# Performance work log

Hardware: AMD Instinct MI355X
Metric: run time of the kernel (lower is better)

## Reference

```python
import jax, jax.numpy as jnp
import numpy as np

EPS_CB = 1e-6   # ConvBlock BN eps (partial(nn.BatchNorm2d, eps=1e-6))
EPS_BN = 1e-5   # default nn.BatchNorm2d / BatchNorm1d eps


def conv2d(x, w, stride=1, pad=0):
    return jax.lax.conv_general_dilated(
        x, w, (stride, stride), [(pad, pad), (pad, pad)],
        dimension_numbers=('NCHW', 'OIHW', 'NCHW'))


def bn2d(x, g, b, m, v, eps):
    inv = (g / jnp.sqrt(v + eps)).reshape(1, -1, 1, 1)
    return (x - m.reshape(1, -1, 1, 1)) * inv + b.reshape(1, -1, 1, 1)


def setup_inputs() -> dict:
    key = jax.random.key(0)
    ks = iter(jax.random.split(key, 40))
    B, C, H, W = 16, 512, 64, 64
    K = 64                 # num_codes (hard-coded to 64 in __init__)
    c4 = C // 4            # bottleneck width in ConvBlock (expansion=4)

    def w_(shape, scale=0.05):
        return jax.random.normal(next(ks), shape, jnp.float32) * scale

    def bnp(n):
        return (jax.random.uniform(next(ks), (n,), jnp.float32, 0.5, 1.5),  # gamma
                w_((n,), 0.05),                                            # beta
                w_((n,), 0.05),                                            # running mean
                jax.random.uniform(next(ks), (n,), jnp.float32, 0.5, 1.5)) # running var

    g1, b1, m1, v1 = bnp(c4)
    g2, b2, m2, v2 = bnp(c4)
    g3, b3, m3, v3 = bnp(C)
    gr, br, mr, vr = bnp(C)
    gl, bl, ml, vl = bnp(C)
    ge, be, me, ve = bnp(K)

    std = 1.0 / np.sqrt(K * C)
    inp = {
        'x': jax.random.normal(next(ks), (B, C, H, W), jnp.float32),
        # ConvBlock
        'w1': w_((c4, C, 1, 1)), 'g1': g1, 'b1': b1, 'm1': m1, 'v1': v1,
        'w2': w_((c4, c4, 3, 3)), 'g2': g2, 'b2': b2, 'm2': m2, 'v2': v2,
        'w3': w_((C, c4, 1, 1)), 'g3': g3, 'b3': b3, 'm3': m3, 'v3': v3,
        'wr': w_((C, C, 1, 1)), 'gr': gr, 'br': br, 'mr': mr, 'vr': vr,
        # LVC 1x1 conv + BN2d
        'wl': w_((C, C, 1, 1)), 'gl': gl, 'bl': bl, 'ml': ml, 'vl': vl,
        # Encoding
        'codewords': jax.random.uniform(next(ks), (K, C), jnp.float32, -std, std),
        'scale': jax.random.uniform(next(ks), (K,), jnp.float32, -1.0, 0.0),
        # BN1d over codes
        'ge': ge, 'be': be, 'me': me, 've': ve,
        # fc gate
        'wfc': w_((C, C)), 'bfc': w_((C,), 0.05),
    }
    return inp


def lvc_forward(x, w1, g1, b1, m1, v1, w2, g2, b2, m2, v2, w3, g3, b3, m3, v3,
                wr, gr, br, mr, vr, wl, gl, bl, ml, vl, codewords, scale,
                ge, be, me, ve, wfc, bfc):
    # ---- ConvBlock (bottleneck with 1x1 residual), eval-mode BN ----
    h = jax.nn.relu(bn2d(conv2d(x, w1), g1, b1, m1, v1, EPS_CB))
    h = jax.nn.relu(bn2d(conv2d(h, w2, pad=1), g2, b2, m2, v2, EPS_CB))
    h = jax.nn.relu(bn2d(conv2d(h, w3), g3, b3, m3, v3, EPS_CB))
    res = bn2d(conv2d(x, wr), gr, br, mr, vr, EPS_CB)
    x1 = h + res                                   # (B, C, H, W)

    # ---- LVC: 1x1 conv + BN + ReLU ----
    y = jax.nn.relu(bn2d(conv2d(x1, wl), gl, bl, ml, vl, EPS_BN))

    # ---- Encoding: scaled L2 -> softmax over codes -> aggregate ----
    B, C, H, W = y.shape
    xf = y.reshape(B, C, H * W).transpose(0, 2, 1)     # (B, N, C)
    x_sq = jnp.sum(xf * xf, axis=-1, keepdims=True)    # (B, N, 1)
    c_sq = jnp.sum(codewords * codewords, axis=-1)     # (K,)
    xc = jnp.einsum('bnc,kc->bnk', xf, codewords)      # (B, N, K)
    dist = scale * (x_sq - 2.0 * xc + c_sq)            # (B, N, K)
    A = jax.nn.softmax(dist, axis=2)                   # assignment weights
    # sum_n A[b,n,k] * (x[b,n,:] - codewords[k,:])  -> (B, K, C)
    enc = jnp.einsum('bnk,bnc->bkc', A, xf) - A.sum(axis=1)[..., None] * codewords

    # ---- BN1d over num_codes dim + ReLU + mean over codes ----
    inv = (ge / jnp.sqrt(ve + EPS_BN)).reshape(1, -1, 1)
    enc = (enc - me.reshape(1, -1, 1)) * inv + be.reshape(1, -1, 1)
    en = jax.nn.relu(enc).mean(axis=1)                 # (B, C)

    # ---- SE-style gate ----
    gam = jax.nn.sigmoid(en @ wfc.T + bfc)             # (B, C)
    gate = gam.reshape(B, C, 1, 1)
    return jax.nn.relu(x1 + x1 * gate)


def reference(x, w1, g1, b1, m1, v1, w2, g2, b2, m2, v2, w3, g3, b3, m3, v3,
              wr, gr, br, mr, vr, wl, gl, bl, ml, vl, codewords, scale,
              ge, be, me, ve, wfc, bfc):
    return lvc_forward(x, w1, g1, b1, m1, v1, w2, g2, b2, m2, v2,
                       w3, g3, b3, m3, v3, wr, gr, br, mr, vr,
                       wl, gl, bl, ml, vl, codewords, scale,
                       ge, be, me, ve, wfc, bfc)
```

## Files before the change

### kernel.cpp

```cpp
#include <hip/hip_runtime.h>
#include <math.h>

typedef float f32x4 __attribute__((ext_vector_type(4)));
typedef short s16x8 __attribute__((ext_vector_type(8)));
typedef unsigned short u16x4 __attribute__((ext_vector_type(4)));

#define HW 4096
#define CCH 512
#define NK 64
#define EPAD 136

#define C_XB   0ULL
#define C_H2   67108864ULL
#define C_H1P  83886080ULL
#define C_X1B  83886080ULL
#define C_YB   0ULL
#define C_AHI  67108864ULL
#define C_ALO  75497472ULL
#define C_ASUM 150994944ULL
#define C_GAM  150999040ULL
#define C_MISC 151031808ULL
#define C_W1F  151048192ULL
#define C_W2F  151179264ULL
#define C_W3B  151474176ULL
#define C_WRB  151605248ULL
#define C_WLB  152129536ULL
#define C_PE   152653824ULL
#define C_CWH  161042432ULL
#define C_CWL  161107968ULL

#define MS_S1 0
#define MS_T1 128
#define MS_S2 256
#define MS_T2 384
#define MS_S3 512
#define MS_T3 1024
#define MS_SR 1536
#define MS_TR 2048
#define MS_SL 2560
#define MS_TL 3072
#define MS_SE 3584
#define MS_TE 3648
#define MS_CSQ 3712

__device__ __forceinline__ float b2f(unsigned short u) {
  unsigned int x = ((unsigned int)u) << 16;
  return __builtin_bit_cast(float, x);
}
__device__ __forceinline__ unsigned short f2b(float f) {
  unsigned int i = __builtin_bit_cast(unsigned int, f);
  i += 0x7fffu + ((i >> 16) & 1u);
  return (unsigned short)(i >> 16);
}

__global__ void prep_kernel(
    const float* __restrict__ g1, const float* __restrict__ b1, const float* __restrict__ m1, const float* __restrict__ v1,
    const float* __restrict__ g2, const float* __restrict__ b2, const float* __restrict__ m2, const float* __restrict__ v2,
    const float* __restrict__ g3, const float* __restrict__ b3, const float* __restrict__ m3, const float* __restrict__ v3,
    const float* __restrict__ gr, const float* __restrict__ br, const float* __restrict__ mr, const float* __restrict__ vr,
    const float* __restrict__ gl, const float* __restrict__ bl, const float* __restrict__ ml, const float* __restrict__ vl,
    const float* __restrict__ ge, const float* __restrict__ be, const float* __restrict__ me, const float* __restrict__ ve,
    const float* __restrict__ cw, float* __restrict__ misc)
{
  const int t = threadIdx.x;
  if (t < 128) {
    float s = g1[t] * rsqrtf(v1[t] + 1e-6f);
    misc[MS_S1 + t] = s; misc[MS_T1 + t] = b1[t] - m1[t] * s;
    s = g2[t] * rsqrtf(v2[t] + 1e-6f);
    misc[MS_S2 + t] = s; misc[MS_T2 + t] = b2[t] - m2[t] * s;
  }
  for (int c = t; c < 512; c += 256) {
    float s = g3[c] * rsqrtf(v3[c] + 1e-6f);
    misc[MS_S3 + c] = s; misc[MS_T3 + c] = b3[c] - m3[c] * s;
    s = gr[c] * rsqrtf(vr[c] + 1e-6f);
    misc[MS_SR + c] = s; misc[MS_TR + c] = br[c] - mr[c] * s;
    s = gl[c] * rsqrtf(vl[c] + 1e-5f);
    misc[MS_SL + c] = s; misc[MS_TL + c] = bl[c] - ml[c] * s;
  }
  if (t < 64) {
    float s = ge[t] * rsqrtf(ve[t] + 1e-5f);
    misc[MS_SE + t] = s; misc[MS_TE + t] = be[t] - me[t] * s;
    float acc = 0.f;
    for (int c = 0; c < 512; ++c) { float v = cw[t * 512 + c]; acc += v * v; }
    misc[MS_CSQ + t] = acc;
  }
}

__global__ void fold_bf16_kernel(const float* __restrict__ w, const float* __restrict__ s,
                                 unsigned short* __restrict__ out, int total, int kper)
{
  int i = blockIdx.x * 256 + threadIdx.x;
  if (i < total) out[i] = f2b(w[i] * s[i / kper]);
}

__global__ void fold_w2_kernel(const float* __restrict__ w2, const float* __restrict__ s,
                               unsigned short* __restrict__ out)
{
  int j = blockIdx.x * 256 + threadIdx.x;
  if (j < 147456) {
    int m = j / 1152, r = j - m * 1152;
    int tp = r >> 7, ci = r & 127;
    out[j] = f2b(w2[m * 1152 + ci * 9 + tp] * s[m]);
  }
}

__global__ void fold_cw_kernel(const float* __restrict__ cw,
                               unsigned short* __restrict__ ch, unsigned short* __restrict__ cl)
{
  int i = blockIdx.x * 256 + threadIdx.x;
  if (i < 32768) {
    const float v = cw[i];
    const unsigned short hi = f2b(v);
    ch[i] = hi;
    cl[i] = f2b(v - b2f(hi));
  }
}

__global__ __launch_bounds__(256) void tr_kernel(const float* __restrict__ x,
                                                 unsigned short* __restrict__ xb)
{
  __shared__ float T[64][65];
  const int b = blockIdx.z, c0 = blockIdx.y * 64, n0 = blockIdx.x * 64;
  const int t = threadIdx.x;
  const int rr = t >> 4, cc = (t & 15) * 4;
#pragma unroll
  for (int rep = 0; rep < 4; ++rep) {
    const int cr = rep * 16 + rr;
    const float4 v = *(const float4*)(x + ((size_t)(b * 512 + c0 + cr)) * 4096 + n0 + cc);
    T[cr][cc + 0] = v.x; T[cr][cc + 1] = v.y; T[cr][cc + 2] = v.z; T[cr][cc + 3] = v.w;
  }
  __syncthreads();
#pragma unroll
  for (int rep = 0; rep < 4; ++rep) {
    const int nr = rep * 16 + rr;
    u16x4 o;
    o[0] = f2b(T[cc + 0][nr]); o[1] = f2b(T[cc + 1][nr]);
    o[2] = f2b(T[cc + 2][nr]); o[3] = f2b(T[cc + 3][nr]);
    *(u16x4*)(xb + ((size_t)(b * 4096 + n0 + nr)) * 512 + c0 + cc) = o;
  }
}

template<int BMODE>
__device__ __forceinline__ void run_phase(
    const unsigned short* __restrict__ Wp,
    const unsigned short* __restrict__ Xb,
    const int K, const int tid, const int n0,
    unsigned short* __restrict__ As, unsigned short* __restrict__ Bs,
    f32x4 acc[4][4])
{
  const int lane = tid & 63;
  const int wv = tid >> 6, wm = wv >> 1, wn = wv & 1;

  const int ko = tid & 3;
  const int r0 = tid >> 2;
  const int r1 = 64 + r0;

  const unsigned short* aS0 = Wp + (size_t)r0 * K + ko * 8;
  const unsigned short* aS1 = Wp + (size_t)r1 * K + ko * 8;
  const int slot0 = (((r0 >> 4) * 64) + ko * 16 + (r0 & 15)) * 8;
  const int slot1 = (((r1 >> 4) * 64) + ko * 16 + (r1 & 15)) * 8;

  const unsigned short* bS0 = nullptr;
  const unsigned short* bS1 = nullptr;
  size_t bBase0 = 0, bBase1 = 0;
  if constexpr (BMODE == 0) {
    bS0 = Xb + (size_t)(n0 + r0) * K + ko * 8;
    bS1 = Xb + (size_t)(n0 + r1) * K + ko * 8;
  } else {
    const int pg0 = n0 + r0, pg1 = n0 + r1;
    bBase0 = (size_t)((pg0 >> 6) * 66 + (pg0 & 63)) * 128 + ko * 8;
    bBase1 = (size_t)((pg1 >> 6) * 66 + (pg1 & 63)) * 128 + ko * 8;
  }

  s16x8 a0, a1, b0, b1;
  auto LOADC = [&](int kt) {
    __builtin_memcpy(&a0, aS0 + kt, 16);
    __builtin_memcpy(&a1, aS1 + kt, 16);
    if constexpr (BMODE == 0) {
      __builtin_memcpy(&b0, bS0 + kt, 16);
      __builtin_memcpy(&b1, bS1 + kt, 16);
    } else {
      const int tap = kt >> 7;
      const int ky = tap / 3, kx = tap - ky * 3;
      const int off = (ky * 66 + kx) * 128 + (kt & 127);
      __builtin_memcpy(&b0, Xb + bBase0 + off, 16);
      __builtin_memcpy(&b1, Xb + bBase1 + off, 16);
    }
  };

  LOADC(0);
  *(s16x8*)(As + slot0) = a0; *(s16x8*)(As + slot1) = a1;
  *(s16x8*)(Bs + slot0) = b0; *(s16x8*)(Bs + slot1) = b1;
  __syncthreads();

  int cur = 0;
  for (int kt = 0; kt < K; kt += 32) {
    const bool more = (kt + 32) < K;
    if (more) LOADC(kt + 32);

    const unsigned short* Ac = As + cur * 4096;
    const unsigned short* Bc = Bs + cur * 4096;
    s16x8 afr[4], bfr[4];
#pragma unroll
    for (int i = 0; i < 4; ++i)
      afr[i] = *(const s16x8*)(Ac + (size_t)((wm * 4 + i) * 64 + lane) * 8);
#pragma unroll
    for (int j = 0; j < 4; ++j)
      bfr[j] = *(const s16x8*)(Bc + (size_t)((wn * 4 + j) * 64 + lane) * 8);
#pragma unroll
    for (int i = 0; i < 4; ++i)
#pragma unroll
      for (int j = 0; j < 4; ++j)
        acc[i][j] = __builtin_amdgcn_mfma_f32_16x16x32_bf16(afr[i], bfr[j], acc[i][j], 0, 0, 0);

    if (more) {
      const int nx = (cur ^ 1) * 4096;
      *(s16x8*)(As + nx + slot0) = a0; *(s16x8*)(As + nx + slot1) = a1;
      *(s16x8*)(Bs + nx + slot0) = b0; *(s16x8*)(Bs + nx + slot1) = b1;
    }
    __syncthreads();
    cur ^= 1;
  }
}

template<int BMODE, bool DUAL>
__global__ __launch_bounds__(256) void mgemm_kernel(
    const unsigned short* __restrict__ W0, const unsigned short* __restrict__ X0,
    const int K0, const long long xbs0,
    const unsigned short* __restrict__ W1, const unsigned short* __restrict__ X1,
    const int Kp1, const long long xbs1,
    const float* __restrict__ biasMid, const float* __restrict__ biasOut,
    const int omode, const int reluF, const int ldm,
    unsigned short* __restrict__ outB, const long long obsB)
{
  __shared__ __align__(16) unsigned short smem[128 * EPAD];
  unsigned short* As = smem;
  unsigned short* Bs = smem + 8192;

  const int tid = threadIdx.x;
  const int b = blockIdx.z;
  const int n0 = blockIdx.x * 128;
  const int m0 = blockIdx.y * 128;
  const int lane = tid & 63, wv = tid >> 6, wm = wv >> 1, wn = wv & 1;
  const int q = lane >> 4, mm = lane & 15;

  f32x4 acc[4][4];
#pragma unroll
  for (int i = 0; i < 4; ++i)
#pragma unroll
    for (int j = 0; j < 4; ++j) acc[i][j] = (f32x4){0.f, 0.f, 0.f, 0.f};

  run_phase<BMODE>(W0 + (size_t)m0 * K0, X0 + (size_t)b * xbs0, K0, tid, n0, As, Bs, acc);

  if constexpr (DUAL) {
#pragma unroll
    for (int i = 0; i < 4; ++i) {
      const int mb = m0 + wm * 64 + i * 16 + q * 4;
#pragma unroll
      for (int r = 0; r < 4; ++r) {
        const float bm = biasMid[mb + r];
#pragma unroll
        for (int j = 0; j < 4; ++j) acc[i][j][r] = fmaxf(acc[i][j][r] + bm, 0.f);
      }
    }
    run_phase<0>(W1 + (size_t)m0 * Kp1, X1 + (size_t)b * xbs1, Kp1, tid, n0, As, Bs, acc);
  }

  __syncthreads();
  if (omode == 3) {
#pragma unroll
    for (int i = 0; i < 4; ++i) {
      const int chb = wm * 64 + i * 16 + q * 4;
#pragma unroll
      for (int r = 0; r < 4; ++r) {
        const float bo = biasOut[m0 + chb + r];
#pragma unroll
        for (int j = 0; j < 4; ++j) {
          const int px = wn * 64 + j * 16 + mm;
          float v = acc[i][j][r] + bo;
          if (reluF) v = fmaxf(v, 0.f);
          smem[(size_t)(chb + r) * EPAD + px] = f2b(v);
        }
      }
    }
    __syncthreads();
    const int ch = tid >> 1, half = tid & 1;
    const unsigned short* src = smem + (size_t)ch * EPAD + half * 64;
    unsigned short* dst = outB + (size_t)b * obsB + (size_t)(m0 + ch) * HW + n0 + half * 64;
#pragma unroll
    for (int r = 0; r < 8; ++r) {
      s16x8 v;
      __builtin_memcpy(&v, src + r * 8, 16);
      *(s16x8*)(dst + r * 8) = v;
    }
  } else {
#pragma unroll
    for (int i = 0; i < 4; ++i) {
      const int chb = wm * 64 + i * 16 + q * 4;
      float bo[4];
#pragma unroll
      for (int r = 0; r < 4; ++r) bo[r] = biasOut[m0 + chb + r];
#pragma unroll
      for (int j = 0; j < 4; ++j) {
        const int px = wn * 64 + j * 16 + mm;
        u16x4 o;
#pragma unroll
        for (int r = 0; r < 4; ++r) {
          float v = acc[i][j][r] + bo[r];
          if (reluF) v = fmaxf(v, 0.f);
          o[r] = f2b(v);
        }
        *(u16x4*)(smem + (size_t)px * EPAD + chb) = o;
      }
    }
    __syncthreads();
    const int px = tid >> 1, half = tid & 1;
    const unsigned short* src = smem + (size_t)px * EPAD + half * 64;
    size_t dstoff;
    if (omode == 1) {
      dstoff = (size_t)b * obsB + (size_t)(n0 + px) * ldm + m0 + half * 64;
    } else {
      const int hp = ((n0 + px) >> 6) + 1, wp = ((n0 + px) & 63) + 1;
      dstoff = (size_t)b * obsB + ((size_t)hp * 66 + wp) * 128 + m0 + half * 64;
    }
    unsigned short* dst = outB + dstoff;
#pragma unroll
    for (int r = 0; r < 8; ++r) {
      s16x8 v;
      __builtin_memcpy(&v, src + r * 8, 16);
      *(s16x8*)(dst + r * 8) = v;
    }
  }
}

__global__ __launch_bounds__(256) void assign_mfma_kernel(
    const unsigned short* __restrict__ Yv,
    const unsigned short* __restrict__ cwh, const unsigned short* __restrict__ cwl,
    const float* __restrict__ scale, const float* __restrict__ misc,
    unsigned short* __restrict__ Ahi, unsigned short* __restrict__ Alo)
{
  __shared__ __align__(16) unsigned short Bt[64][36];
  __shared__ float xpart[64][33];
  __shared__ float dist[64][65];
  __shared__ float red[4][64];
  __shared__ float xsq[64];
  __shared__ float scl[64];
  __shared__ float csq[64];
  const int tid = threadIdx.x;
  const int b = blockIdx.y;
  const int n0 = blockIdx.x * 64;
  const int lane = tid & 63, wv = tid >> 6;
  const int q = lane >> 4, mm = lane & 15;
  if (tid < 64) { scl[tid] = scale[tid]; csq[tid] = misc[MS_CSQ + tid]; }

  const int g = tid >> 5, ci = tid & 31;
  const unsigned short* ySrc = Yv + (size_t)b * CCH * HW + (size_t)ci * HW + n0 + g * 8;
  const unsigned short* ahP = cwh + (size_t)(wv * 16 + mm) * 512 + q * 8;
  const unsigned short* alP = cwl + (size_t)(wv * 16 + mm) * 512 + q * 8;

  f32x4 acc[4];
#pragma unroll
  for (int j = 0; j < 4; ++j) acc[j] = (f32x4){0.f, 0.f, 0.f, 0.f};
  float xp[8] = {0.f, 0.f, 0.f, 0.f, 0.f, 0.f, 0.f, 0.f};

  for (int kc = 0; kc < 16; ++kc) {
    s16x8 v8;
    __builtin_memcpy(&v8, ySrc + (size_t)(kc * 32) * HW, 16);
    s16x8 ah, al;
    __builtin_memcpy(&ah, ahP + kc * 32, 16);
    __builtin_memcpy(&al, alP + kc * 32, 16);
    __syncthreads();
#pragma unroll
    for (int e = 0; e < 8; ++e) {
      Bt[g * 8 + e][ci] = (unsigned short)v8[e];
      const float f = b2f((unsigned short)v8[e]);
      xp[e] += f * f;
    }
    __syncthreads();
#pragma unroll
    for (int j = 0; j < 4; ++j) {
      s16x8 bf;
      __builtin_memcpy(&bf, &Bt[j * 16 + mm][q * 8], 16);
      acc[j] = __builtin_amdgcn_mfma_f32_16x16x32_bf16(ah, bf, acc[j], 0, 0, 0);
      acc[j] = __builtin_amdgcn_mfma_f32_16x16x32_bf16(al, bf, acc[j], 0, 0, 0);
    }
  }

  __syncthreads();
#pragma unroll
  for (int e = 0; e < 8; ++e) xpart[g * 8 + e][ci] = xp[e];
  __syncthreads();
  {
    const int px = tid >> 2, part = tid & 3;
    float s = 0.f;
#pragma unroll
    for (int u = 0; u < 8; ++u) s += xpart[px][part * 8 + u];
    red[part][px] = s;
  }
  __syncthreads();
  if (tid < 64) xsq[tid] = red[0][tid] + red[1][tid] + red[2][tid] + red[3][tid];
  __syncthreads();

#pragma unroll
  for (int j = 0; j < 4; ++j) {
    const int n = j * 16 + mm;
#pragma unroll
    for (int r = 0; r < 4; ++r) {
      const int k = wv * 16 + q * 4 + r;
      dist[k][n] = scl[k] * (xsq[n] - 2.f * acc[j][r] + csq[k]);
    }
  }
  __syncthreads();

  const int qq = tid >> 6, n = tid & 63;
  float mx = -3.0e38f;
#pragma unroll
  for (int kk = 0; kk < 16; ++kk) mx = fmaxf(mx, dist[qq * 16 + kk][n]);
  red[qq][n] = mx;
  __syncthreads();
  mx = fmaxf(fmaxf(red[0][n], red[1][n]), fmaxf(red[2][n], red[3][n]));
  __syncthreads();
  float sum = 0.f;
#pragma unroll
  for (int kk = 0; kk < 16; ++kk) {
    const float e = __expf(dist[qq * 16 + kk][n] - mx);
    dist[qq * 16 + kk][n] = e;
    sum += e;
  }
  red[qq][n] = sum;
  __syncthreads();
  sum = red[0][n] + red[1][n] + red[2][n] + red[3][n];
  const float inv = 1.f / sum;
  const size_t base = (size_t)b * NK * HW + n0 + n;
#pragma unroll
  for (int kk = 0; kk < 16; ++kk) {
    const float a = dist[qq * 16 + kk][n] * inv;
    const unsigned short hi = f2b(a);
    const float rem = a - b2f(hi);
    Ahi[base + (size_t)(qq * 16 + kk) * HW] = hi;
    Alo[base + (size_t)(qq * 16 + kk) * HW] = f2b(rem);
  }
}

__global__ void asum_kernel(const unsigned short* __restrict__ Ahi,
                            const unsigned short* __restrict__ Alo, float* __restrict__ asum)
{
  const int bk = blockIdx.x;
  const unsigned short* __restrict__ rh = Ahi + (size_t)bk * HW;
  const unsigned short* __restrict__ rl = Alo + (size_t)bk * HW;
  const int t = threadIdx.x;
  float p = 0.f;
  for (int i = t * 8; i < HW; i += 2048) {
    s16x8 h, l;
    __builtin_memcpy(&h, rh + i, 16);
    __builtin_memcpy(&l, rl + i, 16);
#pragma unroll
    for (int e = 0; e < 8; ++e)
      p += b2f((unsigned short)h[e]) + b2f((unsigned short)l[e]);
  }
  __shared__ float sm[256];
  sm[t] = p;
  __syncthreads();
  for (int s = 128; s > 0; s >>= 1) {
    if (t < s) sm[t] += sm[t + s];
    __syncthreads();
  }
  if (t == 0) asum[bk] = sm[0];
}

__global__ __launch_bounds__(256) void enc_mfma_kernel(
    const unsigned short* __restrict__ Ahi, const unsigned short* __restrict__ Alo,
    const unsigned short* __restrict__ Yv, float* __restrict__ pe)
{
  __shared__ __align__(16) unsigned short AHs[2048];
  __shared__ __align__(16) unsigned short ALs[2048];
  __shared__ __align__(16) unsigned short Bs[4096];
  const int tid = threadIdx.x;
  const int ncol = blockIdx.x, nc = blockIdx.y, b = blockIdx.z;
  const int lane = tid & 63, wv = tid >> 6;
  const int q = lane >> 4, mm = lane & 15;

  const int ko = tid & 3;
  const int r  = tid >> 2;
  const size_t aoff = ((size_t)b * NK + r) * HW + nc * 1024 + ko * 8;
  const unsigned short* ahS = Ahi + aoff;
  const unsigned short* alS = Alo + aoff;
  const int slotA = (((r >> 4) * 64) + ko * 16 + (r & 15)) * 8;
  const unsigned short* b0S = Yv + ((size_t)b * CCH + ncol * 128 + r) * HW + nc * 1024 + ko * 8;
  const unsigned short* b1S = b0S + (size_t)64 * HW;
  const int slotB0 = (((r >> 4) * 64) + ko * 16 + (r & 15)) * 8;
  const int slotB1 = ((((r + 64) >> 4) * 64) + ko * 16 + (r & 15)) * 8;

  f32x4 acc[4][2];
#pragma unroll
  for (int i = 0; i < 4; ++i)
#pragma unroll
    for (int j = 0; j < 2; ++j) acc[i][j] = (f32x4){0.f, 0.f, 0.f, 0.f};

  for (int kt = 0; kt < 1024; kt += 32) {
    s16x8 ah, al, y0, y1;
    __builtin_memcpy(&ah, ahS + kt, 16);
    __builtin_memcpy(&al, alS + kt, 16);
    __builtin_memcpy(&y0, b0S + kt, 16);
    __builtin_memcpy(&y1, b1S + kt, 16);
    __syncthreads();
    *(s16x8*)(AHs + slotA) = ah;
    *(s16x8*)(ALs + slotA) = al;
    *(s16x8*)(Bs + slotB0) = y0;
    *(s16x8*)(Bs + slotB1) = y1;
    __syncthreads();

    s16x8 afh[4], afl[4], bfr[2];
#pragma unroll
    for (int i = 0; i < 4; ++i) {
      afh[i] = *(const s16x8*)(AHs + (size_t)(i * 64 + lane) * 8);
      afl[i] = *(const s16x8*)(ALs + (size_t)(i * 64 + lane) * 8);
    }
#pragma unroll
    for (int j = 0; j < 2; ++j)
      bfr[j] = *(const s16x8*)(Bs + (size_t)((wv * 2 + j) * 64 + lane) * 8);
#pragma unroll
    for (int i = 0; i < 4; ++i)
#pragma unroll
      for (int j = 0; j < 2; ++j) {
        acc[i][j] = __builtin_amdgcn_mfma_f32_16x16x32_bf16(afh[i], bfr[j], acc[i][j], 0, 0, 0);
        acc[i][j] = __builtin_amdgcn_mfma_f32_16x16x32_bf16(afl[i], bfr[j], acc[i][j], 0, 0, 0);
      }
  }

  float* __restrict__ peb = pe + ((size_t)(b * 4 + nc) * NK) * CCH;
#pragma unroll
  for (int i = 0; i < 4; ++i)
#pragma unroll
    for (int j = 0; j < 2; ++j) {
      const int c = ncol * 128 + (wv * 2 + j) * 16 + mm;
#pragma unroll
      for (int rr = 0; rr < 4; ++rr) {
        const int k = i * 16 + q * 4 + rr;
        peb[(size_t)k * CCH + c] = acc[i][j][rr];
      }
    }
}

__global__ __launch_bounds__(256) void engate_kernel(
    const float* __restrict__ pe, const float* __restrict__ asum, const float* __restrict__ cw,
    const float* __restrict__ misc, const float* __restrict__ wfc, const float* __restrict__ bfc,
    float* __restrict__ gam)
{
  const int b = blockIdx.x;
  const int t = threadIdx.x;
  __shared__ float asum_s[64], se_s[64], te_s[64];
  __shared__ __align__(16) float en_s[512];
  if (t < 64) {
    asum_s[t] = asum[b * 64 + t];
    se_s[t]   = misc[MS_SE + t];
    te_s[t]   = misc[MS_TE + t];
  }
  __syncthreads();
  for (int rep = 0; rep < 2; ++rep) {
    const int c = t + rep * 256;
    float en = 0.f;
    const float* __restrict__ peb = pe + (size_t)b * 4 * NK * CCH + c;
    for (int k = 0; k < 64; ++k) {
      const float ps = peb[(size_t)k * CCH] + peb[(size_t)(64 + k) * CCH] +
                       peb[(size_t)(128 + k) * CCH] + peb[(size_t)(192 + k) * CCH];
      float v = ps - asum_s[k] * cw[k * 512 + c];
      v = v * se_s[k] + te_s[k];
      en += fmaxf(v, 0.f);
    }
    en_s[c] = en * (1.f / 64.f);
  }
  __syncthreads();
  for (int rep = 0; rep < 2; ++rep) {
    const int i = t + rep * 256;
    float a = bfc[i];
    const float4* __restrict__ wrow = (const float4*)(wfc + (size_t)i * 512);
    const float4* __restrict__ ev = (const float4*)en_s;
    for (int j = 0; j < 128; ++j) {
      const float4 w4 = wrow[j];
      const float4 e4 = ev[j];
      a += w4.x * e4.x + w4.y * e4.y + w4.z * e4.z + w4.w * e4.w;
    }
    gam[b * 512 + i] = 1.f / (1.f + __expf(-a));
  }
}

__global__ __launch_bounds__(256) void fingate_kernel(
    const unsigned short* __restrict__ x1b, const float* __restrict__ gam,
    float* __restrict__ out)
{
  __shared__ float T[64][65];
  const int b = blockIdx.z, c0 = blockIdx.y * 64, n0 = blockIdx.x * 64;
  const int t = threadIdx.x;
  const int rr = t >> 4, cc = (t & 15) * 4;
#pragma unroll
  for (int rep = 0; rep < 4; ++rep) {
    const int pr = rep * 16 + rr;
    u16x4 v = *(const u16x4*)(x1b + ((size_t)(b * 4096 + n0 + pr)) * 512 + c0 + cc);
    T[cc + 0][pr] = b2f(v[0]);
    T[cc + 1][pr] = b2f(v[1]);
    T[cc + 2][pr] = b2f(v[2]);
    T[cc + 3][pr] = b2f(v[3]);
  }
  __syncthreads();
#pragma unroll
  for (int rep = 0; rep < 4; ++rep) {
    const int cr = rep * 16 + rr;
    const float g = 1.f + gam[b * 512 + c0 + cr];
    float4 o;
    o.x = fmaxf(T[cr][cc + 0] * g, 0.f);
    o.y = fmaxf(T[cr][cc + 1] * g, 0.f);
    o.z = fmaxf(T[cr][cc + 2] * g, 0.f);
    o.w = fmaxf(T[cr][cc + 3] * g, 0.f);
    *(float4*)(out + ((size_t)(b * 512 + c0 + cr)) * 4096 + n0 + cc) = o;
  }
}

extern "C" void kernel_launch(void* const* d_in, const int* in_sizes, int n_in,
                              void* d_out, int out_size, void* d_ws, size_t ws_size,
                              hipStream_t stream)
{
  const float* x  = (const float*)d_in[0];
  const float* w1 = (const float*)d_in[1];
  const float* g1 = (const float*)d_in[2];
  const float* b1 = (const float*)d_in[3];
  const float* m1 = (const float*)d_in[4];
  const float* v1 = (const float*)d_in[5];
  const float* w2 = (const float*)d_in[6];
  const float* g2 = (const float*)d_in[7];
  const float* b2 = (const float*)d_in[8];
  const float* m2 = (const float*)d_in[9];
  const float* v2 = (const float*)d_in[10];
  const float* w3 = (const float*)d_in[11];
  const float* g3 = (const float*)d_in[12];
  const float* b3 = (const float*)d_in[13];
  const float* m3 = (const float*)d_in[14];
  const float* v3 = (const float*)d_in[15];
  const float* wr = (const float*)d_in[16];
  const float* gr = (const float*)d_in[17];
  const float* br = (const float*)d_in[18];
  const float* mr = (const float*)d_in[19];
  const float* vr = (const float*)d_in[20];
  const float* wl = (const float*)d_in[21];
  const float* gl = (const float*)d_in[22];
  const float* bl = (const float*)d_in[23];
  const float* ml = (const float*)d_in[24];
  const float* vl = (const float*)d_in[25];
  const float* cw = (const float*)d_in[26];
  const float* scale = (const float*)d_in[27];
  const float* ge = (const float*)d_in[28];
  const float* be = (const float*)d_in[29];
  const float* me = (const float*)d_in[30];
  const float* ve = (const float*)d_in[31];
  const float* wfc = (const float*)d_in[32];
  const float* bfc = (const float*)d_in[33];

  char* wsb = (char*)d_ws;
  unsigned short* xb  = (unsigned short*)(wsb + C_XB);
  unsigned short* h2  = (unsigned short*)(wsb + C_H2);
  unsigned short* h1p = (unsigned short*)(wsb + C_H1P);
  unsigned short* x1b = (unsigned short*)(wsb + C_X1B);
  unsigned short* yb  = (unsigned short*)(wsb + C_YB);
  unsigned short* Ahi = (unsigned short*)(wsb + C_AHI);
  unsigned short* Alo = (unsigned short*)(wsb + C_ALO);
  float* pe   = (float*)(wsb + C_PE);
  float* asum = (float*)(wsb + C_ASUM);
  float* gam  = (float*)(wsb + C_GAM);
  float* misc = (float*)(wsb + C_MISC);
  unsigned short* w1f = (unsigned short*)(wsb + C_W1F);
  unsigned short* w2f = (unsigned short*)(wsb + C_W2F);
  unsigned short* w3b = (unsigned short*)(wsb + C_W3B);
  unsigned short* wrb = (unsigned short*)(wsb + C_WRB);
  unsigned short* wlb = (unsigned short*)(wsb + C_WLB);
  unsigned short* cwh = (unsigned short*)(wsb + C_CWH);
  unsigned short* cwl = (unsigned short*)(wsb + C_CWL);

  prep_kernel<<<1, 256, 0, stream>>>(g1, b1, m1, v1, g2, b2, m2, v2, g3, b3, m3, v3,
                                     gr, br, mr, vr, gl, bl, ml, vl, ge, be, me, ve,
                                     cw, misc);
  fold_bf16_kernel<<<256, 256, 0, stream>>>(w1, misc + MS_S1, w1f, 65536, 512);
  fold_w2_kernel<<<576, 256, 0, stream>>>(w2, misc + MS_S2, w2f);
  fold_bf16_kernel<<<256, 256, 0, stream>>>(w3, misc + MS_S3, w3b, 65536, 128);
  fold_bf16_kernel<<<1024, 256, 0, stream>>>(wr, misc + MS_SR, wrb, 262144, 512);
  fold_bf16_kernel<<<1024, 256, 0, stream>>>(wl, misc + MS_SL, wlb, 262144, 512);
  fold_cw_kernel<<<128, 256, 0, stream>>>(cw, cwh, cwl);

  tr_kernel<<<dim3(64, 8, 16), 256, 0, stream>>>(x, xb);
  hipMemsetAsync(h1p, 0, 17842176, stream);

  mgemm_kernel<0, false><<<dim3(32, 1, 16), 256, 0, stream>>>(
      w1f, xb, 512, 4096LL * 512, nullptr, nullptr, 0, 0,
      nullptr, misc + MS_T1, 0, 1, 128, h1p, 4356LL * 128);
  mgemm_kernel<1, false><<<dim3(32, 1, 16), 256, 0, stream>>>(
      w2f, h1p, 1152, 4356LL * 128, nullptr, nullptr, 0, 0,
      nullptr, misc + MS_T2, 1, 1, 128, h2, 4096LL * 128);
  mgemm_kernel<0, true><<<dim3(32, 4, 16), 256, 0, stream>>>(
      w3b, h2, 128, 4096LL * 128, wrb, xb, 512, 4096LL * 512,
      misc + MS_T3, misc + MS_TR, 1, 0, 512, x1b, 4096LL * 512);
  mgemm_kernel<0, false><<<dim3(32, 4, 16), 256, 0, stream>>>(
      wlb, x1b, 512, 4096LL * 512, nullptr, nullptr, 0, 0,
      nullptr, misc + MS_TL, 3, 1, 0, yb, 512LL * 4096);

  assign_mfma_kernel<<<dim3(64, 16), 256, 0, stream>>>(yb, cwh, cwl, scale, misc, Ahi, Alo);
  asum_kernel<<<1024, 256, 0, stream>>>(Ahi, Alo, asum);
  enc_mfma_kernel<<<dim3(4, 4, 16), 256, 0, stream>>>(Ahi, Alo, yb, pe);
  engate_kernel<<<16, 256, 0, stream>>>(pe, asum, cw, misc, wfc, bfc, gam);
  fingate_kernel<<<dim3(64, 8, 16), 256, 0, stream>>>(x1b, gam, (float*)d_out);
}
```

Before: 428.3 us.

## Drop bf16 hi/lo split for codewords and assignments, fuse asum into assign

Removes the low-order bf16 correction terms for the codewords and the soft-assignment matrix, halving the MFMA count in the assign and encode kernels and cutting the A-matrix memory traffic in half. The separate asum reduction kernel is deleted. The assign kernel now reduces assignment sums per wavefront with shuffles and accumulates them through atomics into a buffer zeroed by a new memset. The trade is lower numerical precision in the distance and encoding computations, plus atomic contention on asum.

```diff
diff --git a/kernel.cpp b/kernel.cpp
--- a/kernel.cpp
+++ b/kernel.cpp
@@ -16,7 +16,6 @@
 #define C_X1B  83886080ULL
 #define C_YB   0ULL
 #define C_AHI  67108864ULL
-#define C_ALO  75497472ULL
 #define C_ASUM 150994944ULL
 #define C_GAM  150999040ULL
 #define C_MISC 151031808ULL
@@ -27,7 +26,6 @@
 #define C_WLB  152129536ULL
 #define C_PE   152653824ULL
 #define C_CWH  161042432ULL
-#define C_CWL  161107968ULL
 
 #define MS_S1 0
 #define MS_T1 128
@@ -104,16 +102,10 @@
   }
 }
 
-__global__ void fold_cw_kernel(const float* __restrict__ cw,
-                               unsigned short* __restrict__ ch, unsigned short* __restrict__ cl)
+__global__ void fold_cw_kernel(const float* __restrict__ cw, unsigned short* __restrict__ ch)
 {
   int i = blockIdx.x * 256 + threadIdx.x;
-  if (i < 32768) {
-    const float v = cw[i];
-    const unsigned short hi = f2b(v);
-    ch[i] = hi;
-    cl[i] = f2b(v - b2f(hi));
-  }
+  if (i < 32768) ch[i] = f2b(cw[i]);
 }
 
 __global__ __launch_bounds__(256) void tr_kernel(const float* __restrict__ x,
@@ -335,9 +327,9 @@
 
 __global__ __launch_bounds__(256) void assign_mfma_kernel(
     const unsigned short* __restrict__ Yv,
-    const unsigned short* __restrict__ cwh, const unsigned short* __restrict__ cwl,
+    const unsigned short* __restrict__ cwh,
     const float* __restrict__ scale, const float* __restrict__ misc,
-    unsigned short* __restrict__ Ahi, unsigned short* __restrict__ Alo)
+    unsigned short* __restrict__ Ahi, float* __restrict__ asum)
 {
   __shared__ __align__(16) unsigned short Bt[64][36];
   __shared__ float xpart[64][33];
@@ -356,7 +348,6 @@
   const int g = tid >> 5, ci = tid & 31;
   const unsigned short* ySrc = Yv + (size_t)b * CCH * HW + (size_t)ci * HW + n0 + g * 8;
   const unsigned short* ahP = cwh + (size_t)(wv * 16 + mm) * 512 + q * 8;
-  const unsigned short* alP = cwl + (size_t)(wv * 16 + mm) * 512 + q * 8;
 
   f32x4 acc[4];
 #pragma unroll
@@ -366,9 +357,8 @@
   for (int kc = 0; kc < 16; ++kc) {
     s16x8 v8;
     __builtin_memcpy(&v8, ySrc + (size_t)(kc * 32) * HW, 16);
-    s16x8 ah, al;
+    s16x8 ah;
     __builtin_memcpy(&ah, ahP + kc * 32, 16);
-    __builtin_memcpy(&al, alP + kc * 32, 16);
     __syncthreads();
 #pragma unroll
     for (int e = 0; e < 8; ++e) {
@@ -382,7 +372,6 @@
       s16x8 bf;
       __builtin_memcpy(&bf, &Bt[j * 16 + mm][q * 8], 16);
       acc[j] = __builtin_amdgcn_mfma_f32_16x16x32_bf16(ah, bf, acc[j], 0, 0, 0);
-      acc[j] = __builtin_amdgcn_mfma_f32_16x16x32_bf16(al, bf, acc[j], 0, 0, 0);
     }
   }
 
@@ -435,45 +424,19 @@
 #pragma unroll
   for (int kk = 0; kk < 16; ++kk) {
     const float a = dist[qq * 16 + kk][n] * inv;
-    const unsigned short hi = f2b(a);
-    const float rem = a - b2f(hi);
-    Ahi[base + (size_t)(qq * 16 + kk) * HW] = hi;
-    Alo[base + (size_t)(qq * 16 + kk) * HW] = f2b(rem);
-  }
-}
-
-__global__ void asum_kernel(const unsigned short* __restrict__ Ahi,
-                            const unsigned short* __restrict__ Alo, float* __restrict__ asum)
-{
-  const int bk = blockIdx.x;
-  const unsigned short* __restrict__ rh = Ahi + (size_t)bk * HW;
-  const unsigned short* __restrict__ rl = Alo + (size_t)bk * HW;
-  const int t = threadIdx.x;
-  float p = 0.f;
-  for (int i = t * 8; i < HW; i += 2048) {
-    s16x8 h, l;
-    __builtin_memcpy(&h, rh + i, 16);
-    __builtin_memcpy(&l, rl + i, 16);
-#pragma unroll
-    for (int e = 0; e < 8; ++e)
-      p += b2f((unsigned short)h[e]) + b2f((unsigned short)l[e]);
-  }
-  __shared__ float sm[256];
-  sm[t] = p;
-  __syncthreads();
-  for (int s = 128; s > 0; s >>= 1) {
-    if (t < s) sm[t] += sm[t + s];
-    __syncthreads();
-  }
-  if (t == 0) asum[bk] = sm[0];
+    Ahi[base + (size_t)(qq * 16 + kk) * HW] = f2b(a);
+    float ra = a;
+#pragma unroll
+    for (int off = 32; off >= 1; off >>= 1) ra += __shfl_down(ra, off, 64);
+    if (lane == 0) atomicAdd(&asum[b * 64 + qq * 16 + kk], ra);
+  }
 }
 
 __global__ __launch_bounds__(256) void enc_mfma_kernel(
-    const unsigned short* __restrict__ Ahi, const unsigned short* __restrict__ Alo,
+    const unsigned short* __restrict__ Ahi,
     const unsigned short* __restrict__ Yv, float* __restrict__ pe)
 {
   __shared__ __align__(16) unsigned short AHs[2048];
-  __shared__ __align__(16) unsigned short ALs[2048];
   __shared__ __align__(16) unsigned short Bs[4096];
   const int tid = threadIdx.x;
   const int ncol = blockIdx.x, nc = blockIdx.y, b = blockIdx.z;
@@ -484,7 +447,6 @@
   const int r  = tid >> 2;
   const size_t aoff = ((size_t)b * NK + r) * HW + nc * 1024 + ko * 8;
   const unsigned short* ahS = Ahi + aoff;
-  const unsigned short* alS = Alo + aoff;
   const int slotA = (((r >> 4) * 64) + ko * 16 + (r & 15)) * 8;
   const unsigned short* b0S = Yv + ((size_t)b * CCH + ncol * 128 + r) * HW + nc * 1024 + ko * 8;
   const unsigned short* b1S = b0S + (size_t)64 * HW;
@@ -498,34 +460,28 @@
     for (int j = 0; j < 2; ++j) acc[i][j] = (f32x4){0.f, 0.f, 0.f, 0.f};
 
   for (int kt = 0; kt < 1024; kt += 32) {
-    s16x8 ah, al, y0, y1;
+    s16x8 ah, y0, y1;
     __builtin_memcpy(&ah, ahS + kt, 16);
-    __builtin_memcpy(&al, alS + kt, 16);
     __builtin_memcpy(&y0, b0S + kt, 16);
     __builtin_memcpy(&y1, b1S + kt, 16);
     __syncthreads();
     *(s16x8*)(AHs + slotA) = ah;
-    *(s16x8*)(ALs + slotA) = al;
     *(s16x8*)(Bs + slotB0) = y0;
     *(s16x8*)(Bs + slotB1) = y1;
     __syncthreads();
 
-    s16x8 afh[4], afl[4], bfr[2];
-#pragma unroll
-    for (int i = 0; i < 4; ++i) {
+    s16x8 afh[4], bfr[2];
+#pragma unroll
+    for (int i = 0; i < 4; ++i)
       afh[i] = *(const s16x8*)(AHs + (size_t)(i * 64 + lane) * 8);
-      afl[i] = *(const s16x8*)(ALs + (size_t)(i * 64 + lane) * 8);
-    }
 #pragma unroll
     for (int j = 0; j < 2; ++j)
       bfr[j] = *(const s16x8*)(Bs + (size_t)((wv * 2 + j) * 64 + lane) * 8);
 #pragma unroll
     for (int i = 0; i < 4; ++i)
 #pragma unroll
-      for (int j = 0; j < 2; ++j) {
+      for (int j = 0; j < 2; ++j)
         acc[i][j] = __builtin_amdgcn_mfma_f32_16x16x32_bf16(afh[i], bfr[j], acc[i][j], 0, 0, 0);
-        acc[i][j] = __builtin_amdgcn_mfma_f32_16x16x32_bf16(afl[i], bfr[j], acc[i][j], 0, 0, 0);
-      }
   }
 
   float* __restrict__ peb = pe + ((size_t)(b * 4 + nc) * NK) * CCH;
@@ -662,7 +618,6 @@
   unsigned short* x1b = (unsigned short*)(wsb + C_X1B);
   unsigned short* yb  = (unsigned short*)(wsb + C_YB);
   unsigned short* Ahi = (unsigned short*)(wsb + C_AHI);
-  unsigned short* Alo = (unsigned short*)(wsb + C_ALO);
   float* pe   = (float*)(wsb + C_PE);
   float* asum = (float*)(wsb + C_ASUM);
   float* gam  = (float*)(wsb + C_GAM);
@@ -673,7 +628,6 @@
   unsigned short* wrb = (unsigned short*)(wsb + C_WRB);
   unsigned short* wlb = (unsigned short*)(wsb + C_WLB);
   unsigned short* cwh = (unsigned short*)(wsb + C_CWH);
-  unsigned short* cwl = (unsigned short*)(wsb + C_CWL);
 
   prep_kernel<<<1, 256, 0, stream>>>(g1, b1, m1, v1, g2, b2, m2, v2, g3, b3, m3, v3,
                                      gr, br, mr, vr, gl, bl, ml, vl, ge, be, me, ve,
@@ -683,10 +637,11 @@
   fold_bf16_kernel<<<256, 256, 0, stream>>>(w3, misc + MS_S3, w3b, 65536, 128);
   fold_bf16_kernel<<<1024, 256, 0, stream>>>(wr, misc + MS_SR, wrb, 262144, 512);
   fold_bf16_kernel<<<1024, 256, 0, stream>>>(wl, misc + MS_SL, wlb, 262144, 512);
-  fold_cw_kernel<<<128, 256, 0, stream>>>(cw, cwh, cwl);
+  fold_cw_kernel<<<128, 256, 0, stream>>>(cw, cwh);
 
   tr_kernel<<<dim3(64, 8, 16), 256, 0, stream>>>(x, xb);
   hipMemsetAsync(h1p, 0, 17842176, stream);
+  hipMemsetAsync(asum, 0, 4096, stream);
 
   mgemm_kernel<0, false><<<dim3(32, 1, 16), 256, 0, stream>>>(
       w1f, xb, 512, 4096LL * 512, nullptr, nullptr, 0, 0,
@@ -701,9 +656,8 @@
       wlb, x1b, 512, 4096LL * 512, nullptr, nullptr, 0, 0,
       nullptr, misc + MS_TL, 3, 1, 0, yb, 512LL * 4096);
 
-  assign_mfma_kernel<<<dim3(64, 16), 256, 0, stream>>>(yb, cwh, cwl, scale, misc, Ahi, Alo);
-  asum_kernel<<<1024, 256, 0, stream>>>(Ahi, Alo, asum);
-  enc_mfma_kernel<<<dim3(4, 4, 16), 256, 0, stream>>>(Ahi, Alo, yb, pe);
+  assign_mfma_kernel<<<dim3(64, 16), 256, 0, stream>>>(yb, cwh, scale, misc, Ahi, asum);
+  enc_mfma_kernel<<<dim3(4, 4, 16), 256, 0, stream>>>(Ahi, yb, pe);
   engate_kernel<<<16, 256, 0, stream>>>(pe, asum, cw, misc, wfc, bfc, gam);
   fingate_kernel<<<dim3(64, 8, 16), 256, 0, stream>>>(x1b, gam, (float*)d_out);
 }
```

Measured after the change: 434.9 us. Within noise of the previous version (+1.5%).
